# Kernel tuning notes

Hardware: AMD Instinct MI355X
Metric: run time of the kernel (lower is better)

The kernel has to match this reference:

```python
import jax, jax.numpy as jnp
import numpy as np

N, C, H, W = 4, 32, 384, 1280
DISP_SCALE = 20.0  # realistic disparity magnitudes


def setup_inputs() -> dict:
    key = jax.random.key(0)
    k1, k2 = jax.random.split(key)
    img = jax.random.normal(k1, (N, C, H, W), dtype=jnp.float32)
    disp = jax.random.normal(k2, (N, 1, H, W), dtype=jnp.float32) * DISP_SCALE
    return {"img": img, "disp": disp}


def _warp_bilinear_zeros(img, disp):
    # Faithful translation of Warp1DOp.warp_by_disparity_map with
    # mode='bilinear', padding_mode='zeros', align_corners=True.
    n, c, h, w = img.shape
    # x-coordinate grid minus disparity: (n, 1, h, w)
    x = jnp.arange(w, dtype=img.dtype)[None, None, None, :] - disp
    # zeros padding: clip to [-1, w] then shift by +1 (indices into padded img)
    x = jnp.clip(x, -1.0, jnp.asarray(w, img.dtype)) + 1.0
    # pad coord map and image by one zero column on each side of W
    x = jnp.pad(x, ((0, 0), (0, 0), (0, 0), (1, 1)))          # (n,1,h,w+2)
    imgp = jnp.pad(img, ((0, 0), (0, 0), (0, 0), (1, 1)))      # (n,c,h,w+2)
    x0 = jnp.floor(x).astype(jnp.int32)
    x1 = jnp.ceil(x).astype(jnp.int32)
    dx = x - x0.astype(img.dtype)
    idx_shape = (n, c, h, w + 2)
    v_x0 = jnp.take_along_axis(imgp, jnp.broadcast_to(x0, idx_shape), axis=-1)
    v_x1 = jnp.take_along_axis(imgp, jnp.broadcast_to(x1, idx_shape), axis=-1)
    warped = (1.0 - dx) * v_x0 + dx * v_x1
    # strip padding columns
    return warped[:, :, :, 1:-1]


def reference(img, disp):
    return _warp_bilinear_zeros(img, disp)
```

## Files before the change

### kernel.cpp

```cpp
#include <hip/hip_runtime.h>

#define N_ 4
#define C_ 32
#define H_ 384
#define W_ 1280

__global__ __launch_bounds__(256) void warp1d_kernel(
    const float* __restrict__ img,
    const float* __restrict__ disp,
    float* __restrict__ out)
{
    constexpr int W4 = W_ / 4;
    const int gid = blockIdx.x * blockDim.x + threadIdx.x;
    constexpr int total = N_ * H_ * W4;
    if (gid >= total) return;

    const int w4 = gid % W4;
    const int nh = gid / W4;
    const int w0 = w4 * 4;

    const float4 d4 = *(const float4*)(disp + (long)nh * W_ + w0);
    const float dv[4] = {d4.x, d4.y, d4.z, d4.w};

    int   i0[4], i1[4];
    float fx[4];
    bool  m0[4], m1[4];
#pragma unroll
    for (int j = 0; j < 4; ++j) {
        float x = (float)(w0 + j) - dv[j];
        x = fminf(fmaxf(x, -1.0f), (float)W_) + 1.0f;
        const float xf = floorf(x);
        const float xc = ceilf(x);
        fx[j] = x - xf;
        const int a = (int)xf - 1;
        const int b = (int)xc - 1;
        m0[j] = (unsigned)a < (unsigned)W_;
        m1[j] = (unsigned)b < (unsigned)W_;
        i0[j] = m0[j] ? a : 0;
        i1[j] = m1[j] ? b : 0;
    }

    const int  n = nh / H_;
    const int  h = nh % H_;
    const long rowbase = ((long)n * C_ * H_ + h) * W_;

#pragma unroll 4
    for (int c = 0; c < C_; ++c) {
        const float* __restrict__ r = img + rowbase + (long)c * (H_ * W_);
        float4 o;
        float* op = (float*)&o;
#pragma unroll
        for (int j = 0; j < 4; ++j) {
            const float v0 = m0[j] ? r[i0[j]] : 0.0f;
            const float v1 = m1[j] ? r[i1[j]] : 0.0f;
            op[j] = (1.0f - fx[j]) * v0 + fx[j] * v1;
        }
        *(float4*)(out + rowbase + (long)c * (H_ * W_) + w0) = o;
    }
}

extern "C" void kernel_launch(void* const* d_in, const int* in_sizes, int n_in,
                              void* d_out, int out_size, void* d_ws, size_t ws_size,
                              hipStream_t stream) {
    const float* img  = (const float*)d_in[0];
    const float* disp = (const float*)d_in[1];
    float* out = (float*)d_out;

    constexpr int total   = N_ * H_ * (W_ / 4);
    constexpr int block   = 256;
    constexpr int grid    = (total + block - 1) / block;

    warp1d_kernel<<<grid, block, 0, stream>>>(img, disp, out);
}
```

Baseline: 442.4 us.

## Stage image rows into LDS with async global_load_lds double buffering

Assigns one block per image row and copies each channel's row into shared memory using the async global-to-LDS load, double-buffered across channels. The bilinear gathers then read from LDS instead of scattered global reads. The goal is to replace uncoalesced global gathers with coalesced streaming loads. The cost is a block-wide barrier per channel and a dependence on correct async-load synchronisation.

```diff
diff --git a/kernel.cpp b/kernel.cpp
--- a/kernel.cpp
+++ b/kernel.cpp
@@ -5,19 +5,25 @@
 #define H_ 384
 #define W_ 1280
 
-__global__ __launch_bounds__(256) void warp1d_kernel(
+__device__ __forceinline__ void stage16(const float* g, float* l) {
+    __builtin_amdgcn_global_load_lds(
+        (const __attribute__((address_space(1))) void*)g,
+        (__attribute__((address_space(3))) void*)l, 16, 0, 0);
+}
+
+__global__ __launch_bounds__(320) void warp1d_kernel(
     const float* __restrict__ img,
     const float* __restrict__ disp,
     float* __restrict__ out)
 {
-    constexpr int W4 = W_ / 4;
-    const int gid = blockIdx.x * blockDim.x + threadIdx.x;
-    constexpr int total = N_ * H_ * W4;
-    if (gid >= total) return;
+    __shared__ float buf[2][W_];
 
-    const int w4 = gid % W4;
-    const int nh = gid / W4;
-    const int w0 = w4 * 4;
+    const int tid  = threadIdx.x;
+    const int nh   = blockIdx.x;
+    const int w0   = tid * 4;
+    const int lane = tid & 63;
+    const int wave = tid >> 6;
+    const int chunk = wave * 256 + lane * 4;
 
     const float4 d4 = *(const float4*)(disp + (long)nh * W_ + w0);
     const float dv[4] = {d4.x, d4.y, d4.z, d4.w};
@@ -43,10 +49,20 @@
     const int  n = nh / H_;
     const int  h = nh % H_;
     const long rowbase = ((long)n * C_ * H_ + h) * W_;
+    const float* gsrc = img + rowbase + chunk;
+    float*       gdst = out + rowbase + w0;
 
-#pragma unroll 4
+    stage16(gsrc, &buf[0][wave * 256]);
+    gsrc += (long)H_ * W_;
+    __syncthreads();
+
+#pragma unroll 2
     for (int c = 0; c < C_; ++c) {
-        const float* __restrict__ r = img + rowbase + (long)c * (H_ * W_);
+        if (c + 1 < C_) {
+            stage16(gsrc, &buf[(c + 1) & 1][wave * 256]);
+            gsrc += (long)H_ * W_;
+        }
+        const float* __restrict__ r = buf[c & 1];
         float4 o;
         float* op = (float*)&o;
 #pragma unroll
@@ -55,7 +71,9 @@
             const float v1 = m1[j] ? r[i1[j]] : 0.0f;
             op[j] = (1.0f - fx[j]) * v0 + fx[j] * v1;
         }
-        *(float4*)(out + rowbase + (long)c * (H_ * W_) + w0) = o;
+        *(float4*)gdst = o;
+        gdst += (long)H_ * W_;
+        __syncthreads();
     }
 }
 
@@ -66,9 +84,8 @@
     const float* disp = (const float*)d_in[1];
     float* out = (float*)d_out;
 
-    constexpr int total   = N_ * H_ * (W_ / 4);
-    constexpr int block   = 256;
-    constexpr int grid    = (total + block - 1) / block;
+    constexpr int grid  = N_ * H_;
+    constexpr int block = 320;
 
     warp1d_kernel<<<grid, block, 0, stream>>>(img, disp, out);
 }
```

New measurement: 426.9 us. 3.5% less time.
